# Kernel tuning notes

Measured on AMD Instinct MI355X. Metric: run time of the kernel, lower is better.

## Reference

```python
import jax, jax.numpy as jnp
import numpy as np

NUM_HEADS = 12
EPS = 1e-6


def _rms_norm(x, w):
    # RMSNorm over the full channel dim (applied before head split), fp32 math
    return x * jax.lax.rsqrt(jnp.mean(x * x, axis=-1, keepdims=True) + EPS) * w


def _rope_apply(t, F, H, W, freqs):
    # t: [B, S, n, d] with S == F*H*W; freqs: [1024, d//2] angles
    B, S, n, d = t.shape
    c = d // 2
    s0 = c - 2 * (c // 3)  # temporal split (22 when d=128)
    s1 = c // 3            # spatial splits (21, 21)
    f0, f1, f2 = freqs[:, :s0], freqs[:, s0:s0 + s1], freqs[:, s0 + s1:]
    ang = jnp.concatenate([
        jnp.broadcast_to(f0[:F, None, None, :], (F, H, W, s0)),
        jnp.broadcast_to(f1[None, :H, None, :], (F, H, W, s1)),
        jnp.broadcast_to(f2[None, None, :W, :], (F, H, W, s1)),
    ], axis=-1).reshape(S, c)                      # [S, c]
    cos = jnp.cos(ang)[None, :, None, :]           # [1, S, 1, c]
    sin = jnp.sin(ang)[None, :, None, :]
    tp = t.reshape(B, S, n, c, 2)
    te, to = tp[..., 0], tp[..., 1]                # complex (real, imag) pairs
    rot = jnp.stack([te * cos - to * sin, te * sin + to * cos], axis=-1)
    return rot.reshape(B, S, n, d)


def reference(x, seq_lens, grid_sizes, freqs, Wq, bq, Wk, bk, Wv, bv, Wo, bo, norm_q_w, norm_k_w):
    B, S, C = x.shape
    n = NUM_HEADS
    d = C // n
    gs = np.asarray(grid_sizes)[0]
    F, H, W = int(gs[0]), int(gs[1]), int(gs[2])  # static: L == F*H*W, same per sample

    q = _rms_norm(x @ Wq.T + bq, norm_q_w).reshape(B, S, n, d)
    k = _rms_norm(x @ Wk.T + bk, norm_k_w).reshape(B, S, n, d)
    v = (x @ Wv.T + bv).reshape(B, S, n, d)

    q = _rope_apply(q, F, H, W, freqs)
    k = _rope_apply(k, F, H, W, freqs)

    scale = 1.0 / jnp.sqrt(jnp.float32(d))
    scores = jnp.einsum('bqnd,bknd->bnqk', q, k) * scale   # [B, n, S, S]
    kmask = jnp.arange(S)[None, :] < seq_lens[:, None]      # [B, S] valid keys
    scores = jnp.where(kmask[:, None, None, :], scores, -jnp.inf)
    attn = jax.nn.softmax(scores, axis=-1)
    out = jnp.einsum('bnqk,bknd->bqnd', attn, v).reshape(B, S, C)
    return out @ Wo.T + bo


def setup_inputs() -> dict:
    key = jax.random.key(0)
    ks = jax.random.split(key, 10)
    B, F, H, W = 2, 4, 24, 32
    S = F * H * W  # 3072
    C = 1536
    d = C // NUM_HEADS  # 128
    c = d // 2          # 64

    x = jax.random.normal(ks[0], (B, S, C), dtype=jnp.float32)
    seq_lens = jnp.array([S, 2500], dtype=jnp.int32)
    grid_sizes = jnp.array([[F, H, W]] * B, dtype=jnp.int32)

    # rope angles: outer(pos, 1/theta^(2i/dim)) per split [22, 21, 21]
    def rope_params(max_len, dim_k, theta=10000.0):
        inv = 1.0 / (theta ** (np.arange(0, dim_k, 2, dtype=np.float64) / dim_k))
        return np.outer(np.arange(max_len), inv)
    s0 = c - 2 * (c // 3)
    s1 = c // 3
    freqs = jnp.asarray(np.concatenate([
        rope_params(1024, 2 * s0), rope_params(1024, 2 * s1), rope_params(1024, 2 * s1)
    ], axis=1), dtype=jnp.float32)  # [1024, 64]

    std = 0.02
    def lin(k):
        return jax.random.normal(k, (C, C), dtype=jnp.float32) * std
    return {
        'x': x, 'seq_lens': seq_lens, 'grid_sizes': grid_sizes, 'freqs': freqs,
        'Wq': lin(ks[1]), 'bq': jnp.zeros((C,), jnp.float32),
        'Wk': lin(ks[2]), 'bk': jnp.zeros((C,), jnp.float32),
        'Wv': lin(ks[3]), 'bv': jnp.zeros((C,), jnp.float32),
        'Wo': lin(ks[4]), 'bo': jnp.zeros((C,), jnp.float32),
        'norm_q_w': jnp.ones((C,), jnp.float32),
        'norm_k_w': jnp.ones((C,), jnp.float32),
    }
```

## Files before the change

kernel.cpp:

```cpp
#include <hip/hip_runtime.h>
#include <math.h>

#define NB 2
#define SS 3072
#define CC 1536
#define NH 12
#define DH 128
#define NTOK (NB * SS)
#define WE (CC * CC)
#define LOG2E 1.4426950408889634f

typedef __attribute__((ext_vector_type(8))) short short8;
typedef __attribute__((ext_vector_type(4))) float floatx4;

#define GLOAD(g, l) __builtin_amdgcn_global_load_lds( \
    (const __attribute__((address_space(1))) void*)(g), \
    (__attribute__((address_space(3))) void*)(l), 16, 0, 0)

__device__ __forceinline__ unsigned short f2bf(float f) {
    unsigned u = __float_as_uint(f);
    u += 0x7fffu + ((u >> 16) & 1u);
    return (unsigned short)(u >> 16);
}

__global__ __launch_bounds__(256) void cast_all(
    const float* __restrict__ x,
    const float* __restrict__ w0, const float* __restrict__ w1,
    const float* __restrict__ w2, const float* __restrict__ w3,
    unsigned short* __restrict__ o)
{
    const int y = blockIdx.y;
    const float* src = (y < 4) ? x + (size_t)y * WE
                     : (y == 4) ? w0 : (y == 5) ? w1 : (y == 6) ? w2 : w3;
    size_t i = ((size_t)blockIdx.x * 256 + threadIdx.x) * 4;
    float4 v = *(const float4*)&src[i];
    uint2 u;
    u.x = (unsigned)f2bf(v.x) | ((unsigned)f2bf(v.y) << 16);
    u.y = (unsigned)f2bf(v.z) | ((unsigned)f2bf(v.w) << 16);
    *(uint2*)&o[(size_t)y * WE + i] = u;
}

__global__ __launch_bounds__(256) void qkv_gemm(
    const unsigned short* __restrict__ X,
    const unsigned short* __restrict__ Wqb, const unsigned short* __restrict__ Wkb,
    const unsigned short* __restrict__ Wvb,
    const float* __restrict__ bq, const float* __restrict__ bk,
    const float* __restrict__ bv,
    unsigned short* __restrict__ qo, unsigned short* __restrict__ ko,
    unsigned short* __restrict__ vto)
{
    __shared__ unsigned short As[128 * 32];
    __shared__ unsigned short Bs[128 * 32];
    const int tid = threadIdx.x;
    const int w = tid >> 6, l = tid & 63;
    const int jseg = blockIdx.y / 12;
    const unsigned short* Wt = (jseg == 0) ? Wqb : (jseg == 1) ? Wkb : Wvb;
    const float* bias        = (jseg == 0) ? bq  : (jseg == 1) ? bk  : bv;
    unsigned short* Y        = (jseg == 0) ? qo  : (jseg == 1) ? ko  : vto;
    const int i0 = blockIdx.x * 128, j0 = (blockIdx.y % 12) * 128;
    const int srow = tid >> 2;
    const int sk8 = (tid & 3) * 8;

    floatx4 acc[4][4] = {};
    for (int k0 = 0; k0 < CC; k0 += 32) {
        __syncthreads();
        GLOAD(X + (size_t)(i0 + srow) * CC + k0 + sk8,        As + (size_t)tid * 8);
        GLOAD(X + (size_t)(i0 + 64 + srow) * CC + k0 + sk8,   As + (size_t)(256 + tid) * 8);
        GLOAD(Wt + (size_t)(j0 + srow) * CC + k0 + sk8,       Bs + (size_t)tid * 8);
        GLOAD(Wt + (size_t)(j0 + 64 + srow) * CC + k0 + sk8,  Bs + (size_t)(256 + tid) * 8);
        __syncthreads();
        const int wr = (w >> 1) * 64, wc = (w & 1) * 64;
        short8 af[4], bf[4];
        #pragma unroll
        for (int mb = 0; mb < 4; ++mb)
            af[mb] = *(const short8*)&As[(wr + mb * 16 + (l & 15)) * 32 + (l >> 4) * 8];
        #pragma unroll
        for (int nb = 0; nb < 4; ++nb)
            bf[nb] = *(const short8*)&Bs[(wc + nb * 16 + (l & 15)) * 32 + (l >> 4) * 8];
        #pragma unroll
        for (int mb = 0; mb < 4; ++mb)
            #pragma unroll
            for (int nb = 0; nb < 4; ++nb)
                acc[mb][nb] = __builtin_amdgcn_mfma_f32_16x16x32_bf16(
                    af[mb], bf[nb], acc[mb][nb], 0, 0, 0);
    }

    const int wr = (w >> 1) * 64, wc = (w & 1) * 64;
    #pragma unroll
    for (int mb = 0; mb < 4; ++mb)
        #pragma unroll
        for (int nb = 0; nb < 4; ++nb) {
            const int n = j0 + wc + nb * 16 + (l & 15);
            const float bv2 = bias[n];
            const int h = n >> 7, td = n & 127;
            #pragma unroll
            for (int r = 0; r < 4; ++r) {
                const int m = i0 + wr + mb * 16 + (l >> 4) * 4 + r;
                const float val = acc[mb][nb][r] + bv2;
                const int b = (m >= SS) ? 1 : 0;
                const int s = m - b * SS;
                if (jseg < 2)
                    Y[((size_t)(b * NH + h) * SS + s) * DH + td] = f2bf(val);
                else
                    Y[((size_t)(b * NH + h) * DH + td) * SS + s] = f2bf(val);
            }
        }
}

__global__ __launch_bounds__(256) void gemm_o(
    const unsigned short* __restrict__ X, const unsigned short* __restrict__ Wt,
    const float* __restrict__ bias, float* __restrict__ Y)
{
    __shared__ unsigned short As[128 * 32];
    __shared__ unsigned short Bs[128 * 32];
    const int tid = threadIdx.x;
    const int w = tid >> 6, l = tid & 63;
    const int i0 = blockIdx.x * 128, j0 = blockIdx.y * 128;
    const int srow = tid >> 2;
    const int sk8 = (tid & 3) * 8;

    floatx4 acc[4][4] = {};
    for (int k0 = 0; k0 < CC; k0 += 32) {
        __syncthreads();
        GLOAD(X + (size_t)(i0 + srow) * CC + k0 + sk8,        As + (size_t)tid * 8);
        GLOAD(X + (size_t)(i0 + 64 + srow) * CC + k0 + sk8,   As + (size_t)(256 + tid) * 8);
        GLOAD(Wt + (size_t)(j0 + srow) * CC + k0 + sk8,       Bs + (size_t)tid * 8);
        GLOAD(Wt + (size_t)(j0 + 64 + srow) * CC + k0 + sk8,  Bs + (size_t)(256 + tid) * 8);
        __syncthreads();
        const int wr = (w >> 1) * 64, wc = (w & 1) * 64;
        short8 af[4], bf[4];
        #pragma unroll
        for (int mb = 0; mb < 4; ++mb)
            af[mb] = *(const short8*)&As[(wr + mb * 16 + (l & 15)) * 32 + (l >> 4) * 8];
        #pragma unroll
        for (int nb = 0; nb < 4; ++nb)
            bf[nb] = *(const short8*)&Bs[(wc + nb * 16 + (l & 15)) * 32 + (l >> 4) * 8];
        #pragma unroll
        for (int mb = 0; mb < 4; ++mb)
            #pragma unroll
            for (int nb = 0; nb < 4; ++nb)
                acc[mb][nb] = __builtin_amdgcn_mfma_f32_16x16x32_bf16(
                    af[mb], bf[nb], acc[mb][nb], 0, 0, 0);
    }

    const int wr = (w >> 1) * 64, wc = (w & 1) * 64;
    #pragma unroll
    for (int mb = 0; mb < 4; ++mb)
        #pragma unroll
        for (int nb = 0; nb < 4; ++nb) {
            const int n = j0 + wc + nb * 16 + (l & 15);
            const float bv = bias[n];
            #pragma unroll
            for (int r = 0; r < 4; ++r) {
                const int m = i0 + wr + mb * 16 + (l >> 4) * 4 + r;
                Y[(size_t)m * CC + n] = acc[mb][nb][r] + bv;
            }
        }
}

__global__ __launch_bounds__(256) void norm_rope(
    unsigned short* __restrict__ qb, unsigned short* __restrict__ kb,
    const float* __restrict__ nqw, const float* __restrict__ nkw,
    const float* __restrict__ freqs, const int* __restrict__ gsz)
{
    const int bid = blockIdx.x;
    const int which = (bid >= NTOK) ? 1 : 0;
    const int tok = bid - which * NTOK;
    unsigned short* t       = which ? kb : qb;
    const float* wgt        = which ? nkw : nqw;
    const float outscale    = which ? 1.0f : 0.08838834764831845f * LOG2E;
    const int b = tok / SS, s = tok - b * SS;
    const int Hg = gsz[1], Wg = gsz[2];
    const int f = s / (Hg * Wg);
    const int rem = s - f * Hg * Wg;
    const int hh = rem / Wg;
    const int ww = rem - hh * Wg;
    const int tid = threadIdx.x;

    float2 vals[3];
    size_t addrs[3];
    float ss = 0.f;
    #pragma unroll
    for (int kt = 0; kt < 3; ++kt) {
        int p = tid + kt * 256;
        int h = p >> 6, pj = p & 63;
        size_t addr = ((size_t)(b * NH + h) * SS + s) * DH + 2 * pj;
        addrs[kt] = addr;
        unsigned u = *(const unsigned*)&t[addr];
        float2 v;
        v.x = __uint_as_float(u << 16);
        v.y = __uint_as_float(u & 0xffff0000u);
        vals[kt] = v;
        ss += v.x * v.x + v.y * v.y;
    }
    #pragma unroll
    for (int off = 32; off > 0; off >>= 1) ss += __shfl_down(ss, off, 64);
    __shared__ float red[4];
    if ((tid & 63) == 0) red[tid >> 6] = ss;
    __syncthreads();
    const float total = red[0] + red[1] + red[2] + red[3];
    const float rstd = rsqrtf(total * (1.0f / CC) + 1e-6f) * outscale;

    #pragma unroll
    for (int kt = 0; kt < 3; ++kt) {
        int p = tid + kt * 256;
        int h = p >> 6, pj = p & 63;
        int row = (pj < 22) ? f : ((pj < 43) ? hh : ww);
        float ang = freqs[row * 64 + pj];
        float sn, cs;
        sincosf(ang, &sn, &cs);
        int ch = h * DH + 2 * pj;
        float te = vals[kt].x * rstd * wgt[ch];
        float to = vals[kt].y * rstd * wgt[ch + 1];
        unsigned o = (unsigned)f2bf(te * cs - to * sn) |
                     ((unsigned)f2bf(te * sn + to * cs) << 16);
        *(unsigned*)&t[addrs[kt]] = o;
    }
}

__global__ __launch_bounds__(256) void flash_attn_mfma(
    const unsigned short* __restrict__ qg, const unsigned short* __restrict__ kg,
    const unsigned short* __restrict__ vg, const int* __restrict__ seq_lens,
    unsigned short* __restrict__ out)
{
    __shared__ unsigned short Qs[4 * 64 * 32];
    __shared__ unsigned short Ks[4 * 64 * 32];
    __shared__ unsigned short Vs[2 * 128 * 32];

    const int tid = threadIdx.x;
    const int w = tid >> 6, l = tid & 63;
    const int bid = blockIdx.x;
    const int qt  = bid / (NB * NH);
    const int rem0 = bid - qt * (NB * NH);
    const int h = rem0 >> 1;
    const int b = rem0 & 1;
    const int slen = seq_lens[b];
    const int s0 = qt * 64;

    const unsigned short* qbase = qg + ((size_t)(b * NH + h) * SS + s0) * DH;
    const unsigned short* kbase = kg + ((size_t)(b * NH + h) * SS) * DH;
    const unsigned short* vbase = vg + ((size_t)(b * NH + h) * DH) * SS;
    unsigned short* Psw = Qs + (size_t)w * (16 * 72);

    #pragma unroll
    for (int i = 0; i < 4; ++i) {
        int cid = i * 256 + tid;
        int kc = cid >> 8, r2 = cid & 255, row = r2 >> 2, k8 = (r2 & 3) * 8;
        GLOAD(qbase + row * DH + kc * 32 + k8, Qs + (size_t)cid * 8);
    }
    __syncthreads();
    short8 qf[4];
    #pragma unroll
    for (int kc = 0; kc < 4; ++kc)
        qf[kc] = *(const short8*)&Qs[kc * 2048 + (w * 16 + (l & 15)) * 32 + (l >> 4) * 8];

    floatx4 acc[8] = {};
    float lsum[4] = {};
    const int ntiles = (slen + 63) >> 6;

    for (int kt = 0; kt < ntiles; ++kt) {
        __syncthreads();
        #pragma unroll
        for (int i = 0; i < 4; ++i) {
            int cid = i * 256 + tid;
            int kc = cid >> 8, r2 = cid & 255, row = r2 >> 2, k8 = (r2 & 3) * 8;
            GLOAD(kbase + (size_t)(kt * 64 + row) * DH + kc * 32 + k8, Ks + (size_t)cid * 8);
        }
        #pragma unroll
        for (int i = 0; i < 4; ++i) {
            int cid = i * 256 + tid;
            int ks = cid >> 9, r2 = cid & 511, dc = r2 >> 2, k8 = (r2 & 3) * 8;
            GLOAD(vbase + (size_t)dc * SS + kt * 64 + ks * 32 + k8, Vs + (size_t)cid * 8);
        }
        __syncthreads();

        floatx4 sv[4] = {};
        #pragma unroll
        for (int nb = 0; nb < 4; ++nb)
            #pragma unroll
            for (int kc = 0; kc < 4; ++kc) {
                short8 kf = *(const short8*)&Ks[kc * 2048 + (nb * 16 + (l & 15)) * 32 + (l >> 4) * 8];
                sv[nb] = __builtin_amdgcn_mfma_f32_16x16x32_bf16(qf[kc], kf, sv[nb], 0, 0, 0);
            }

        const int valid = slen - kt * 64;
        float pv[4][4];
        if (valid >= 64) {
            #pragma unroll
            for (int nb = 0; nb < 4; ++nb)
                #pragma unroll
                for (int r = 0; r < 4; ++r)
                    pv[nb][r] = exp2f(sv[nb][r]);
        } else {
            #pragma unroll
            for (int nb = 0; nb < 4; ++nb) {
                const int key = nb * 16 + (l & 15);
                #pragma unroll
                for (int r = 0; r < 4; ++r)
                    pv[nb][r] = (key < valid) ? exp2f(sv[nb][r]) : 0.0f;
            }
        }
        #pragma unroll
        for (int r = 0; r < 4; ++r)
            lsum[r] += pv[0][r] + pv[1][r] + pv[2][r] + pv[3][r];

        #pragma unroll
        for (int nb = 0; nb < 4; ++nb)
            #pragma unroll
            for (int r = 0; r < 4; ++r)
                Psw[((l >> 4) * 4 + r) * 72 + nb * 16 + (l & 15)] = f2bf(pv[nb][r]);

        short8 pa[2];
        #pragma unroll
        for (int ks = 0; ks < 2; ++ks)
            pa[ks] = *(const short8*)&Psw[(l & 15) * 72 + ks * 32 + (l >> 4) * 8];
        #pragma unroll
        for (int nb2 = 0; nb2 < 8; ++nb2)
            #pragma unroll
            for (int ks = 0; ks < 2; ++ks) {
                short8 vf = *(const short8*)&Vs[ks * 4096 + (nb2 * 16 + (l & 15)) * 32 + (l >> 4) * 8];
                acc[nb2] = __builtin_amdgcn_mfma_f32_16x16x32_bf16(pa[ks], vf, acc[nb2], 0, 0, 0);
            }
    }

    float rl[4];
    #pragma unroll
    for (int r = 0; r < 4; ++r) {
        float s = lsum[r];
        #pragma unroll
        for (int mm = 1; mm < 16; mm <<= 1) s += __shfl_xor(s, mm, 64);
        rl[r] = 1.0f / s;
    }
    #pragma unroll
    for (int nb2 = 0; nb2 < 8; ++nb2) {
        const int col = h * DH + nb2 * 16 + (l & 15);
        #pragma unroll
        for (int r = 0; r < 4; ++r) {
            const int srow = s0 + w * 16 + (l >> 4) * 4 + r;
            out[((size_t)b * SS + srow) * CC + col] = f2bf(acc[nb2][r] * rl[r]);
        }
    }
}

extern "C" void kernel_launch(void* const* d_in, const int* in_sizes, int n_in,
                              void* d_out, int out_size, void* d_ws, size_t ws_size,
                              hipStream_t stream) {
    const float* x          = (const float*)d_in[0];
    const int*   seq_lens   = (const int*)d_in[1];
    const int*   grid_sizes = (const int*)d_in[2];
    const float* freqs      = (const float*)d_in[3];
    const float* Wq         = (const float*)d_in[4];
    const float* bq         = (const float*)d_in[5];
    const float* Wk         = (const float*)d_in[6];
    const float* bk         = (const float*)d_in[7];
    const float* Wv         = (const float*)d_in[8];
    const float* bv         = (const float*)d_in[9];
    const float* Wo         = (const float*)d_in[10];
    const float* bo         = (const float*)d_in[11];
    const float* nqw        = (const float*)d_in[12];
    const float* nkw        = (const float*)d_in[13];
    float* out = (float*)d_out;

    const size_t TE = (size_t)NTOK * CC;
    unsigned short* xb  = (unsigned short*)d_ws;
    unsigned short* wqb = xb + TE;
    unsigned short* wkb = wqb + WE;
    unsigned short* wvb = wkb + WE;
    unsigned short* wob = wvb + WE;
    unsigned short* qb  = wob + WE;
    unsigned short* kb  = qb + TE;
    unsigned short* vtb = kb + TE;
    unsigned short* ab  = vtb + TE;

    cast_all<<<dim3(WE / 1024, 8), 256, 0, stream>>>(x, Wq, Wk, Wv, Wo, xb);

    qkv_gemm<<<dim3(NTOK / 128, 36), 256, 0, stream>>>(
        xb, wqb, wkb, wvb, bq, bk, bv, qb, kb, vtb);

    norm_rope<<<dim3(2 * NTOK), 256, 0, stream>>>(qb, kb, nqw, nkw, freqs, grid_sizes);

    flash_attn_mfma<<<dim3(NB * NH * (SS / 64)), 256, 0, stream>>>(qb, kb, vtb, seq_lens, ab);

    gemm_o<<<dim3(NTOK / 128, CC / 128), 256, 0, stream>>>(ab, wob, bo, out);
}
```

Before: 574.8 us.

## Swizzle LDS tiles, double flash-attn query tile, precompute rope table

```diff
diff --git a/kernel.cpp b/kernel.cpp
--- a/kernel.cpp
+++ b/kernel.cpp
@@ -21,6 +21,9 @@
     unsigned u = __float_as_uint(f);
     u += 0x7fffu + ((u >> 16) & 1u);
     return (unsigned short)(u >> 16);
+}
+__device__ __forceinline__ int swz(int row, int q) {
+    return row * 4 + (q ^ ((row >> 1) & 3));
 }
 
 __global__ __launch_bounds__(256) void cast_all(
@@ -38,6 +41,23 @@
     u.x = (unsigned)f2bf(v.x) | ((unsigned)f2bf(v.y) << 16);
     u.y = (unsigned)f2bf(v.z) | ((unsigned)f2bf(v.w) << 16);
     *(uint2*)&o[(size_t)y * WE + i] = u;
+}
+
+__global__ __launch_bounds__(256) void rope_table(
+    const float* __restrict__ freqs, const int* __restrict__ gsz,
+    float2* __restrict__ tab)
+{
+    const int id = blockIdx.x * 256 + threadIdx.x;
+    const int s = id >> 6, pj = id & 63;
+    const int Hg = gsz[1], Wg = gsz[2];
+    const int f = s / (Hg * Wg);
+    const int rem = s - f * Hg * Wg;
+    const int hh = rem / Wg;
+    const int ww = rem - hh * Wg;
+    const int row = (pj < 22) ? f : ((pj < 43) ? hh : ww);
+    float sn, cs;
+    sincosf(freqs[row * 64 + pj], &sn, &cs);
+    tab[id] = make_float2(cs, sn);
 }
 
 __global__ __launch_bounds__(256) void qkv_gemm(
@@ -59,24 +79,24 @@
     unsigned short* Y        = (jseg == 0) ? qo  : (jseg == 1) ? ko  : vto;
     const int i0 = blockIdx.x * 128, j0 = (blockIdx.y % 12) * 128;
     const int srow = tid >> 2;
-    const int sk8 = (tid & 3) * 8;
+    const int gk8 = (((tid & 3) ^ ((srow >> 1) & 3))) * 8;
 
     floatx4 acc[4][4] = {};
     for (int k0 = 0; k0 < CC; k0 += 32) {
         __syncthreads();
-        GLOAD(X + (size_t)(i0 + srow) * CC + k0 + sk8,        As + (size_t)tid * 8);
-        GLOAD(X + (size_t)(i0 + 64 + srow) * CC + k0 + sk8,   As + (size_t)(256 + tid) * 8);
-        GLOAD(Wt + (size_t)(j0 + srow) * CC + k0 + sk8,       Bs + (size_t)tid * 8);
-        GLOAD(Wt + (size_t)(j0 + 64 + srow) * CC + k0 + sk8,  Bs + (size_t)(256 + tid) * 8);
+        GLOAD(X + (size_t)(i0 + srow) * CC + k0 + gk8,        As + (size_t)tid * 8);
+        GLOAD(X + (size_t)(i0 + 64 + srow) * CC + k0 + gk8,   As + (size_t)(256 + tid) * 8);
+        GLOAD(Wt + (size_t)(j0 + srow) * CC + k0 + gk8,       Bs + (size_t)tid * 8);
+        GLOAD(Wt + (size_t)(j0 + 64 + srow) * CC + k0 + gk8,  Bs + (size_t)(256 + tid) * 8);
         __syncthreads();
         const int wr = (w >> 1) * 64, wc = (w & 1) * 64;
         short8 af[4], bf[4];
         #pragma unroll
         for (int mb = 0; mb < 4; ++mb)
-            af[mb] = *(const short8*)&As[(wr + mb * 16 + (l & 15)) * 32 + (l >> 4) * 8];
+            af[mb] = *(const short8*)&As[swz(wr + mb * 16 + (l & 15), l >> 4) * 8];
         #pragma unroll
         for (int nb = 0; nb < 4; ++nb)
-            bf[nb] = *(const short8*)&Bs[(wc + nb * 16 + (l & 15)) * 32 + (l >> 4) * 8];
+            bf[nb] = *(const short8*)&Bs[swz(wc + nb * 16 + (l & 15), l >> 4) * 8];
         #pragma unroll
         for (int mb = 0; mb < 4; ++mb)
             #pragma unroll
@@ -117,24 +137,24 @@
     const int w = tid >> 6, l = tid & 63;
     const int i0 = blockIdx.x * 128, j0 = blockIdx.y * 128;
     const int srow = tid >> 2;
-    const int sk8 = (tid & 3) * 8;
+    const int gk8 = (((tid & 3) ^ ((srow >> 1) & 3))) * 8;
 
     floatx4 acc[4][4] = {};
     for (int k0 = 0; k0 < CC; k0 += 32) {
         __syncthreads();
-        GLOAD(X + (size_t)(i0 + srow) * CC + k0 + sk8,        As + (size_t)tid * 8);
-        GLOAD(X + (size_t)(i0 + 64 + srow) * CC + k0 + sk8,   As + (size_t)(256 + tid) * 8);
-        GLOAD(Wt + (size_t)(j0 + srow) * CC + k0 + sk8,       Bs + (size_t)tid * 8);
-        GLOAD(Wt + (size_t)(j0 + 64 + srow) * CC + k0 + sk8,  Bs + (size_t)(256 + tid) * 8);
+        GLOAD(X + (size_t)(i0 + srow) * CC + k0 + gk8,        As + (size_t)tid * 8);
+        GLOAD(X + (size_t)(i0 + 64 + srow) * CC + k0 + gk8,   As + (size_t)(256 + tid) * 8);
+        GLOAD(Wt + (size_t)(j0 + srow) * CC + k0 + gk8,       Bs + (size_t)tid * 8);
+        GLOAD(Wt + (size_t)(j0 + 64 + srow) * CC + k0 + gk8,  Bs + (size_t)(256 + tid) * 8);
         __syncthreads();
         const int wr = (w >> 1) * 64, wc = (w & 1) * 64;
         short8 af[4], bf[4];
         #pragma unroll
         for (int mb = 0; mb < 4; ++mb)
-            af[mb] = *(const short8*)&As[(wr + mb * 16 + (l & 15)) * 32 + (l >> 4) * 8];
+            af[mb] = *(const short8*)&As[swz(wr + mb * 16 + (l & 15), l >> 4) * 8];
         #pragma unroll
         for (int nb = 0; nb < 4; ++nb)
-            bf[nb] = *(const short8*)&Bs[(wc + nb * 16 + (l & 15)) * 32 + (l >> 4) * 8];
+            bf[nb] = *(const short8*)&Bs[swz(wc + nb * 16 + (l & 15), l >> 4) * 8];
         #pragma unroll
         for (int mb = 0; mb < 4; ++mb)
             #pragma unroll
@@ -161,20 +181,15 @@
 __global__ __launch_bounds__(256) void norm_rope(
     unsigned short* __restrict__ qb, unsigned short* __restrict__ kb,
     const float* __restrict__ nqw, const float* __restrict__ nkw,
-    const float* __restrict__ freqs, const int* __restrict__ gsz)
+    const float2* __restrict__ tab)
 {
     const int bid = blockIdx.x;
     const int which = (bid >= NTOK) ? 1 : 0;
     const int tok = bid - which * NTOK;
-    unsigned short* t       = which ? kb : qb;
-    const float* wgt        = which ? nkw : nqw;
-    const float outscale    = which ? 1.0f : 0.08838834764831845f * LOG2E;
+    unsigned short* t    = which ? kb : qb;
+    const float* wgt     = which ? nkw : nqw;
+    const float outscale = which ? 1.0f : 0.08838834764831845f * LOG2E;
     const int b = tok / SS, s = tok - b * SS;
-    const int Hg = gsz[1], Wg = gsz[2];
-    const int f = s / (Hg * Wg);
-    const int rem = s - f * Hg * Wg;
-    const int hh = rem / Wg;
-    const int ww = rem - hh * Wg;
     const int tid = threadIdx.x;
 
     float2 vals[3];
@@ -205,57 +220,57 @@
     for (int kt = 0; kt < 3; ++kt) {
         int p = tid + kt * 256;
         int h = p >> 6, pj = p & 63;
-        int row = (pj < 22) ? f : ((pj < 43) ? hh : ww);
-        float ang = freqs[row * 64 + pj];
-        float sn, cs;
-        sincosf(ang, &sn, &cs);
+        float2 cssn = tab[s * 64 + pj];
         int ch = h * DH + 2 * pj;
         float te = vals[kt].x * rstd * wgt[ch];
         float to = vals[kt].y * rstd * wgt[ch + 1];
-        unsigned o = (unsigned)f2bf(te * cs - to * sn) |
-                     ((unsigned)f2bf(te * sn + to * cs) << 16);
+        unsigned o = (unsigned)f2bf(te * cssn.x - to * cssn.y) |
+                     ((unsigned)f2bf(te * cssn.y + to * cssn.x) << 16);
         *(unsigned*)&t[addrs[kt]] = o;
     }
 }
 
-__global__ __launch_bounds__(256) void flash_attn_mfma(
+__global__ __launch_bounds__(256, 2) void flash_attn_mfma(
     const unsigned short* __restrict__ qg, const unsigned short* __restrict__ kg,
     const unsigned short* __restrict__ vg, const int* __restrict__ seq_lens,
     unsigned short* __restrict__ out)
 {
-    __shared__ unsigned short Qs[4 * 64 * 32];
-    __shared__ unsigned short Ks[4 * 64 * 32];
-    __shared__ unsigned short Vs[2 * 128 * 32];
+    __shared__ unsigned short Qs[128 * 128];
+    __shared__ unsigned short Ks[64 * 128];
+    __shared__ unsigned short Vs[128 * 64];
 
     const int tid = threadIdx.x;
     const int w = tid >> 6, l = tid & 63;
     const int bid = blockIdx.x;
-    const int qt  = bid / (NB * NH);
+    const int qt = bid / (NB * NH);
     const int rem0 = bid - qt * (NB * NH);
     const int h = rem0 >> 1;
     const int b = rem0 & 1;
     const int slen = seq_lens[b];
-    const int s0 = qt * 64;
+    const int s0 = qt * 128;
 
     const unsigned short* qbase = qg + ((size_t)(b * NH + h) * SS + s0) * DH;
     const unsigned short* kbase = kg + ((size_t)(b * NH + h) * SS) * DH;
     const unsigned short* vbase = vg + ((size_t)(b * NH + h) * DH) * SS;
-    unsigned short* Psw = Qs + (size_t)w * (16 * 72);
-
-    #pragma unroll
-    for (int i = 0; i < 4; ++i) {
+    unsigned short* Psw = Qs + (size_t)w * (32 * 72);
+
+    #pragma unroll
+    for (int i = 0; i < 8; ++i) {
         int cid = i * 256 + tid;
-        int kc = cid >> 8, r2 = cid & 255, row = r2 >> 2, k8 = (r2 & 3) * 8;
-        GLOAD(qbase + row * DH + kc * 32 + k8, Qs + (size_t)cid * 8);
+        int kc = cid >> 9, r2 = cid & 511, row = r2 >> 2, sq = r2 & 3;
+        GLOAD(qbase + (size_t)row * DH + kc * 32 + (sq ^ ((row >> 1) & 3)) * 8,
+              Qs + (size_t)cid * 8);
     }
     __syncthreads();
-    short8 qf[4];
-    #pragma unroll
-    for (int kc = 0; kc < 4; ++kc)
-        qf[kc] = *(const short8*)&Qs[kc * 2048 + (w * 16 + (l & 15)) * 32 + (l >> 4) * 8];
-
-    floatx4 acc[8] = {};
-    float lsum[4] = {};
+    short8 qf[2][4];
+    #pragma unroll
+    for (int rb = 0; rb < 2; ++rb)
+        #pragma unroll
+        for (int kc = 0; kc < 4; ++kc)
+            qf[rb][kc] = *(const short8*)&Qs[(kc * 512 + swz(w * 32 + rb * 16 + (l & 15), l >> 4)) * 8];
+
+    floatx4 acc[2][8] = {};
+    float lsum[2][4] = {};
     const int ntiles = (slen + 63) >> 6;
 
     for (int kt = 0; kt < ntiles; ++kt) {
@@ -263,81 +278,98 @@
         #pragma unroll
         for (int i = 0; i < 4; ++i) {
             int cid = i * 256 + tid;
-            int kc = cid >> 8, r2 = cid & 255, row = r2 >> 2, k8 = (r2 & 3) * 8;
-            GLOAD(kbase + (size_t)(kt * 64 + row) * DH + kc * 32 + k8, Ks + (size_t)cid * 8);
+            int kc = cid >> 8, r2 = cid & 255, row = r2 >> 2, sq = r2 & 3;
+            GLOAD(kbase + (size_t)(kt * 64 + row) * DH + kc * 32 + (sq ^ ((row >> 1) & 3)) * 8,
+                  Ks + (size_t)cid * 8);
         }
         #pragma unroll
         for (int i = 0; i < 4; ++i) {
             int cid = i * 256 + tid;
-            int ks = cid >> 9, r2 = cid & 511, dc = r2 >> 2, k8 = (r2 & 3) * 8;
-            GLOAD(vbase + (size_t)dc * SS + kt * 64 + ks * 32 + k8, Vs + (size_t)cid * 8);
-        }
-        __syncthreads();
-
-        floatx4 sv[4] = {};
-        #pragma unroll
-        for (int nb = 0; nb < 4; ++nb)
-            #pragma unroll
-            for (int kc = 0; kc < 4; ++kc) {
-                short8 kf = *(const short8*)&Ks[kc * 2048 + (nb * 16 + (l & 15)) * 32 + (l >> 4) * 8];
-                sv[nb] = __builtin_amdgcn_mfma_f32_16x16x32_bf16(qf[kc], kf, sv[nb], 0, 0, 0);
+            int ks = cid >> 9, r2 = cid & 511, dc = r2 >> 2, sq = r2 & 3;
+            GLOAD(vbase + (size_t)dc * SS + kt * 64 + ks * 32 + (sq ^ ((dc >> 1) & 3)) * 8,
+                  Vs + (size_t)cid * 8);
+        }
+        __syncthreads();
+
+        floatx4 sv[2][4] = {};
+        #pragma unroll
+        for (int kc = 0; kc < 4; ++kc) {
+            short8 kf[4];
+            #pragma unroll
+            for (int nb = 0; nb < 4; ++nb)
+                kf[nb] = *(const short8*)&Ks[(kc * 256 + swz(nb * 16 + (l & 15), l >> 4)) * 8];
+            #pragma unroll
+            for (int rb = 0; rb < 2; ++rb)
+                #pragma unroll
+                for (int nb = 0; nb < 4; ++nb)
+                    sv[rb][nb] = __builtin_amdgcn_mfma_f32_16x16x32_bf16(
+                        qf[rb][kc], kf[nb], sv[rb][nb], 0, 0, 0);
+        }
+
+        const int valid = slen - kt * 64;
+        #pragma unroll
+        for (int rb = 0; rb < 2; ++rb) {
+            if (valid >= 64) {
+                #pragma unroll
+                for (int nb = 0; nb < 4; ++nb)
+                    #pragma unroll
+                    for (int r = 0; r < 4; ++r)
+                        sv[rb][nb][r] = exp2f(sv[rb][nb][r]);
+            } else {
+                #pragma unroll
+                for (int nb = 0; nb < 4; ++nb) {
+                    const int key = nb * 16 + (l & 15);
+                    #pragma unroll
+                    for (int r = 0; r < 4; ++r)
+                        sv[rb][nb][r] = (key < valid) ? exp2f(sv[rb][nb][r]) : 0.0f;
+                }
             }
-
-        const int valid = slen - kt * 64;
-        float pv[4][4];
-        if (valid >= 64) {
+            #pragma unroll
+            for (int r = 0; r < 4; ++r)
+                lsum[rb][r] += sv[rb][0][r] + sv[rb][1][r] + sv[rb][2][r] + sv[rb][3][r];
             #pragma unroll
             for (int nb = 0; nb < 4; ++nb)
                 #pragma unroll
                 for (int r = 0; r < 4; ++r)
-                    pv[nb][r] = exp2f(sv[nb][r]);
-        } else {
-            #pragma unroll
-            for (int nb = 0; nb < 4; ++nb) {
-                const int key = nb * 16 + (l & 15);
+                    Psw[(rb * 16 + (l >> 4) * 4 + r) * 72 + nb * 16 + (l & 15)] =
+                        f2bf(sv[rb][nb][r]);
+        }
+
+        #pragma unroll
+        for (int ks = 0; ks < 2; ++ks) {
+            short8 pa[2];
+            #pragma unroll
+            for (int rb = 0; rb < 2; ++rb)
+                pa[rb] = *(const short8*)&Psw[(rb * 16 + (l & 15)) * 72 + ks * 32 + (l >> 4) * 8];
+            #pragma unroll
+            for (int nb2 = 0; nb2 < 8; ++nb2) {
+                short8 vf = *(const short8*)&Vs[(ks * 512 + swz(nb2 * 16 + (l & 15), l >> 4)) * 8];
                 #pragma unroll
-                for (int r = 0; r < 4; ++r)
-                    pv[nb][r] = (key < valid) ? exp2f(sv[nb][r]) : 0.0f;
+                for (int rb = 0; rb < 2; ++rb)
+                    acc[rb][nb2] = __builtin_amdgcn_mfma_f32_16x16x32_bf16(
+                        pa[rb], vf, acc[rb][nb2], 0, 0, 0);
             }
         }
-        #pragma unroll
-        for (int r = 0; r < 4; ++r)
-            lsum[r] += pv[0][r] + pv[1][r] + pv[2][r] + pv[3][r];
-
-        #pragma unroll
-        for (int nb = 0; nb < 4; ++nb)
-            #pragma unroll
-            for (int r = 0; r < 4; ++r)
-                Psw[((l >> 4) * 4 + r) * 72 + nb * 16 + (l & 15)] = f2bf(pv[nb][r]);
-
-        short8 pa[2];
-        #pragma unroll
-        for (int ks = 0; ks < 2; ++ks)
-            pa[ks] = *(const short8*)&Psw[(l & 15) * 72 + ks * 32 + (l >> 4) * 8];
-        #pragma unroll
-        for (int nb2 = 0; nb2 < 8; ++nb2)
-            #pragma unroll
-            for (int ks = 0; ks < 2; ++ks) {
-                short8 vf = *(const short8*)&Vs[ks * 4096 + (nb2 * 16 + (l & 15)) * 32 + (l >> 4) * 8];
-                acc[nb2] = __builtin_amdgcn_mfma_f32_16x16x32_bf16(pa[ks], vf, acc[nb2], 0, 0, 0);
+    }
+
+    #pragma unroll
+    for (int rb = 0; rb < 2; ++rb) {
+        float rl[4];
+        #pragma unroll
+        for (int r = 0; r < 4; ++r) {
+            float s = lsum[rb][r];
+            #pragma unroll
+            for (int mm = 1; mm < 16; mm <<= 1) s += __shfl_xor(s, mm, 64);
+            rl[r] = 1.0f / s;
+        }
+        #pragma unroll
+        for (int nb2 = 0; nb2 < 8; ++nb2) {
+            const int col = h * DH + nb2 * 16 + (l & 15);
+            #pragma unroll
+            for (int r = 0; r < 4; ++r) {
+                const int srow = s0 + w * 32 + rb * 16 + (l >> 4) * 4 + r;
+                out[((size_t)b * SS + srow) * CC + col] = f2bf(acc[rb][nb2][r] * rl[r]);
             }
-    }
-
-    float rl[4];
-    #pragma unroll
-    for (int r = 0; r < 4; ++r) {
-        float s = lsum[r];
-        #pragma unroll
-        for (int mm = 1; mm < 16; mm <<= 1) s += __shfl_xor(s, mm, 64);
-        rl[r] = 1.0f / s;
-    }
-    #pragma unroll
-    for (int nb2 = 0; nb2 < 8; ++nb2) {
-        const int col = h * DH + nb2 * 16 + (l & 15);
-        #pragma unroll
-        for (int r = 0; r < 4; ++r) {
-            const int srow = s0 + w * 16 + (l >> 4) * 4 + r;
-            out[((size_t)b * SS + srow) * CC + col] = f2bf(acc[nb2][r] * rl[r]);
         }
     }
 }
@@ -371,15 +403,17 @@
     unsigned short* kb  = qb + TE;
     unsigned short* vtb = kb + TE;
     unsigned short* ab  = vtb + TE;
+    float2* tab = (float2*)(ab + TE);
 
     cast_all<<<dim3(WE / 1024, 8), 256, 0, stream>>>(x, Wq, Wk, Wv, Wo, xb);
+    rope_table<<<dim3(SS * 64 / 256), 256, 0, stream>>>(freqs, grid_sizes, tab);
 
     qkv_gemm<<<dim3(NTOK / 128, 36), 256, 0, stream>>>(
         xb, wqb, wkb, wvb, bq, bk, bv, qb, kb, vtb);
 
-    norm_rope<<<dim3(2 * NTOK), 256, 0, stream>>>(qb, kb, nqw, nkw, freqs, grid_sizes);
-
-    flash_attn_mfma<<<dim3(NB * NH * (SS / 64)), 256, 0, stream>>>(qb, kb, vtb, seq_lens, ab);
+    norm_rope<<<dim3(2 * NTOK), 256, 0, stream>>>(qb, kb, nqw, nkw, tab);
+
+    flash_attn_mfma<<<dim3(NB * NH * (SS / 128)), 256, 0, stream>>>(qb, kb, vtb, seq_lens, ab);
 
     gemm_o<<<dim3(NTOK / 128, CC / 128), 256, 0, stream>>>(ab, wob, bo, out);
 }
```

New measurement: 560.0 us. 2.6% less time.
